# Performance work log

Hardware: AMD Instinct MI355X
Metric: run time of the kernel (lower is better)

## Reference

```python
import jax, jax.numpy as jnp
import numpy as np

B, S, D, Q = 8, 4096, 1024, 16  # batch, seq, embed_dim, n_qubits==ffn_dim


def setup_inputs() -> dict:
    key = jax.random.key(0)
    k = jax.random.split(key, 5)
    x = jax.random.normal(k[0], (B, S, D), dtype=jnp.float32)
    W1 = jax.random.normal(k[1], (D, Q), dtype=jnp.float32) * 0.02
    b1 = jnp.zeros((Q,), dtype=jnp.float32)
    theta = jax.random.normal(k[2], (Q,), dtype=jnp.float32)
    W2 = jax.random.normal(k[3], (Q, D), dtype=jnp.float32) * 0.02
    b2 = jnp.zeros((D,), dtype=jnp.float32)
    return {"x": x, "W1": W1, "b1": b1, "theta": theta, "W2": W2, "b2": b2}


def reference(x, W1, b1, theta, W2, b2):
    # linear1 + ReLU (dropout is identity in eval mode)
    h = jax.nn.relu(jnp.einsum("bsd,dq->bsq", x, W1) + b1)  # [B,S,Q] angles
    # QLayer: RY(h_i) then RY(theta_i) on wire i from |0>; rotations on the
    # same wire compose additively and <Z> after RY(a)|0> is cos(a), so
    # MeasureAll(PauliZ) == cos(h + theta) per wire (exact, product state).
    z = jnp.cos(h + theta)  # [B,S,Q]
    # linear2
    return jnp.einsum("bsq,qd->bsd", z, W2) + b2
```

## Files before the change

kernel.cpp:

```cpp
#include <hip/hip_runtime.h>
#include <math.h>
#include <stdint.h>

#define ROWS_TOTAL 32768
#define DDIM 1024
#define QDIM 16

typedef __attribute__((ext_vector_type(8))) short bf16x8;
typedef __attribute__((ext_vector_type(4))) float f32x4;

union ABfrag { uint32_t u[4]; bf16x8 v; };

__device__ __forceinline__ uint32_t packhi(uint32_t a, uint32_t b) {
  return __builtin_amdgcn_perm(b, a, 0x07060302u);
}

#define ZTPB 512
#define ZWPB 8
#define ZNBLOCKS (ROWS_TOTAL / 16)

__global__ __launch_bounds__(ZTPB, 4)
void z_kernel(const float* __restrict__ x, const float* __restrict__ W1,
              const float* __restrict__ b1, const float* __restrict__ theta,
              float* __restrict__ z, int zstride) {
  const int t    = threadIdx.x;
  const int lane = t & 63;
  const int wid  = t >> 6;
  const int g    = lane >> 4;
  const int q5   = lane & 15;

  __shared__ __align__(16) float red[ZWPB][64][4];

  const int row0 = blockIdx.x * 16;
  const int kb   = wid * 128;

  const float bq = b1[q5];
  const float tq = theta[q5];

  float wf[4][8];
#pragma unroll
  for (int s = 0; s < 4; ++s) {
    const float* wp = W1 + (size_t)(kb + 32 * s + 4 * g) * QDIM + q5;
#pragma unroll
    for (int j = 0; j < 4; ++j) wf[s][j] = wp[(size_t)j * QDIM];
#pragma unroll
    for (int j = 0; j < 4; ++j) wf[s][4 + j] = wp[(size_t)(16 + j) * QDIM];
  }

  const float* xl = x + (size_t)(row0 + q5) * DDIM + kb + 4 * g;
  float4 a0[4], a1[4];
#pragma unroll
  for (int s = 0; s < 4; ++s) {
    a0[s] = *reinterpret_cast<const float4*>(xl + 32 * s);
    a1[s] = *reinterpret_cast<const float4*>(xl + 32 * s + 16);
  }

  ABfrag bhi[4], blo[4];
#pragma unroll
  for (int s = 0; s < 4; ++s) {
    uint32_t u[8], lo[8];
#pragma unroll
    for (int j = 0; j < 8; ++j) {
      u[j]  = __float_as_uint(wf[s][j]);
      lo[j] = __float_as_uint(wf[s][j] - __uint_as_float(u[j] & 0xFFFF0000u));
    }
    bhi[s].u[0] = packhi(u[0], u[1]);   bhi[s].u[1] = packhi(u[2], u[3]);
    bhi[s].u[2] = packhi(u[4], u[5]);   bhi[s].u[3] = packhi(u[6], u[7]);
    blo[s].u[0] = packhi(lo[0], lo[1]); blo[s].u[1] = packhi(lo[2], lo[3]);
    blo[s].u[2] = packhi(lo[4], lo[5]); blo[s].u[3] = packhi(lo[6], lo[7]);
  }

  f32x4 acc = {0.f, 0.f, 0.f, 0.f};
#pragma unroll
  for (int s = 0; s < 4; ++s) {
    const float fv[8] = {a0[s].x, a0[s].y, a0[s].z, a0[s].w,
                         a1[s].x, a1[s].y, a1[s].z, a1[s].w};
    uint32_t u[8], lo[8];
#pragma unroll
    for (int j = 0; j < 8; ++j) {
      u[j]  = __float_as_uint(fv[j]);
      lo[j] = __float_as_uint(fv[j] - __uint_as_float(u[j] & 0xFFFF0000u));
    }
    ABfrag ahi, alo;
    ahi.u[0] = packhi(u[0], u[1]);   ahi.u[1] = packhi(u[2], u[3]);
    ahi.u[2] = packhi(u[4], u[5]);   ahi.u[3] = packhi(u[6], u[7]);
    alo.u[0] = packhi(lo[0], lo[1]); alo.u[1] = packhi(lo[2], lo[3]);
    alo.u[2] = packhi(lo[4], lo[5]); alo.u[3] = packhi(lo[6], lo[7]);

    acc = __builtin_amdgcn_mfma_f32_16x16x32_bf16(ahi.v, bhi[s].v, acc, 0, 0, 0);
    acc = __builtin_amdgcn_mfma_f32_16x16x32_bf16(alo.v, bhi[s].v, acc, 0, 0, 0);
    acc = __builtin_amdgcn_mfma_f32_16x16x32_bf16(ahi.v, blo[s].v, acc, 0, 0, 0);
  }

  *reinterpret_cast<f32x4*>(&red[wid][lane][0]) = acc;
  __syncthreads();

  if (wid == 0) {
    f32x4 s0 = *reinterpret_cast<const f32x4*>(&red[0][lane][0]);
#pragma unroll
    for (int w = 1; w < ZWPB; ++w)
      s0 += *reinterpret_cast<const f32x4*>(&red[w][lane][0]);

    const int r0 = g * 4;
#pragma unroll
    for (int i = 0; i < 4; ++i) {
      const float sv = fmaxf(s0[i] + bq, 0.f) + tq;
      z[(size_t)(row0 + r0 + i) * zstride + q5] = __cosf(sv);
    }
  }
}

#define OTPB 256
#define ORPB 16
#define ONBLOCKS (ROWS_TOTAL / ORPB)

__global__ __launch_bounds__(OTPB, 4)
void o_kernel(const float* z, int zstride, const float* __restrict__ W2,
              const float* __restrict__ b2, float* out) {
  const int t   = threadIdx.x;
  const int col = 4 * t;

  float4 w2r[QDIM];
#pragma unroll
  for (int q = 0; q < QDIM; ++q)
    w2r[q] = *reinterpret_cast<const float4*>(W2 + (size_t)q * DDIM + col);
  const float4 bb = *reinterpret_cast<const float4*>(b2 + col);

  const int row0 = blockIdx.x * ORPB;

  const float* zp0 = z + (size_t)row0 * zstride;
  float4 zc0 = *reinterpret_cast<const float4*>(zp0 + 0);
  float4 zc1 = *reinterpret_cast<const float4*>(zp0 + 4);
  float4 zc2 = *reinterpret_cast<const float4*>(zp0 + 8);
  float4 zc3 = *reinterpret_cast<const float4*>(zp0 + 12);

#pragma unroll
  for (int r = 0; r < ORPB; ++r) {
    float4 zn0 = zc0, zn1 = zc1, zn2 = zc2, zn3 = zc3;
    if (r + 1 < ORPB) {
      const float* znp = z + (size_t)(row0 + r + 1) * zstride;
      zn0 = *reinterpret_cast<const float4*>(znp + 0);
      zn1 = *reinterpret_cast<const float4*>(znp + 4);
      zn2 = *reinterpret_cast<const float4*>(znp + 8);
      zn3 = *reinterpret_cast<const float4*>(znp + 12);
    }

    const float zv[16] = {zc0.x, zc0.y, zc0.z, zc0.w,
                          zc1.x, zc1.y, zc1.z, zc1.w,
                          zc2.x, zc2.y, zc2.z, zc2.w,
                          zc3.x, zc3.y, zc3.z, zc3.w};
    float4 acc = bb;
#pragma unroll
    for (int q = 0; q < QDIM; ++q) {
      acc.x = fmaf(zv[q], w2r[q].x, acc.x);
      acc.y = fmaf(zv[q], w2r[q].y, acc.y);
      acc.z = fmaf(zv[q], w2r[q].z, acc.z);
      acc.w = fmaf(zv[q], w2r[q].w, acc.w);
    }
    *reinterpret_cast<float4*>(out + (size_t)(row0 + r) * DDIM + col) = acc;

    zc0 = zn0; zc1 = zn1; zc2 = zn2; zc3 = zn3;
  }
}

extern "C" void kernel_launch(void* const* d_in, const int* in_sizes, int n_in,
                              void* d_out, int out_size, void* d_ws, size_t ws_size,
                              hipStream_t stream) {
  const float* x     = (const float*)d_in[0];
  const float* W1    = (const float*)d_in[1];
  const float* b1    = (const float*)d_in[2];
  const float* theta = (const float*)d_in[3];
  const float* W2    = (const float*)d_in[4];
  const float* b2    = (const float*)d_in[5];
  float* out = (float*)d_out;

  const size_t zbytes = (size_t)ROWS_TOTAL * QDIM * sizeof(float);
  float* zbuf;
  int zstride;
  if (d_ws != nullptr && ws_size >= zbytes) {
    zbuf = (float*)d_ws;
    zstride = QDIM;
  } else {
    zbuf = out;
    zstride = DDIM;
  }

  z_kernel<<<dim3(ZNBLOCKS), dim3(ZTPB), 0, stream>>>(x, W1, b1, theta, zbuf, zstride);
  o_kernel<<<dim3(ONBLOCKS), dim3(OTPB), 0, stream>>>(zbuf, zstride, W2, b2, out);
}
```

Measured before the change: 55.46 us.

## Stage x tile through swizzled LDS for coalesced global loads in z_kernel

```diff
diff --git a/kernel.cpp b/kernel.cpp
--- a/kernel.cpp
+++ b/kernel.cpp
@@ -29,6 +29,7 @@
   const int g    = lane >> 4;
   const int q5   = lane & 15;
 
+  __shared__ __align__(16) float xs[16][DDIM];
   __shared__ __align__(16) float red[ZWPB][64][4];
 
   const int row0 = blockIdx.x * 16;
@@ -47,12 +48,27 @@
     for (int j = 0; j < 4; ++j) wf[s][4 + j] = wp[(size_t)(16 + j) * QDIM];
   }
 
-  const float* xl = x + (size_t)(row0 + q5) * DDIM + kb + 4 * g;
-  float4 a0[4], a1[4];
-#pragma unroll
-  for (int s = 0; s < 4; ++s) {
-    a0[s] = *reinterpret_cast<const float4*>(xl + 32 * s);
-    a1[s] = *reinterpret_cast<const float4*>(xl + 32 * s + 16);
+  float4 st[8];
+  {
+    const int rs = 2 * wid;
+#pragma unroll
+    for (int rr = 0; rr < 2; ++rr) {
+      const float* xp = x + (size_t)(row0 + rs + rr) * DDIM;
+#pragma unroll
+      for (int p = 0; p < 4; ++p)
+        st[rr * 4 + p] =
+            *reinterpret_cast<const float4*>(xp + 4 * (64 * p + lane));
+    }
+#pragma unroll
+    for (int rr = 0; rr < 2; ++rr) {
+      const int r = rs + rr;
+#pragma unroll
+      for (int p = 0; p < 4; ++p) {
+        const int u = 64 * p + lane;
+        *reinterpret_cast<float4*>(&xs[r][4 * (u ^ (r & 7))]) =
+            st[rr * 4 + p];
+      }
+    }
   }
 
   ABfrag bhi[4], blo[4];
@@ -68,6 +84,19 @@
     bhi[s].u[2] = packhi(u[4], u[5]);   bhi[s].u[3] = packhi(u[6], u[7]);
     blo[s].u[0] = packhi(lo[0], lo[1]); blo[s].u[1] = packhi(lo[2], lo[3]);
     blo[s].u[2] = packhi(lo[4], lo[5]); blo[s].u[3] = packhi(lo[6], lo[7]);
+  }
+
+  __syncthreads();
+
+  const int rr = lane & 15;
+  const int ub = 32 * wid;
+  float4 a0[4], a1[4];
+#pragma unroll
+  for (int s = 0; s < 4; ++s) {
+    a0[s] = *reinterpret_cast<const float4*>(
+        &xs[rr][4 * ((ub + 8 * s + g) ^ (rr & 7))]);
+    a1[s] = *reinterpret_cast<const float4*>(
+        &xs[rr][4 * ((ub + 8 * s + 4 + g) ^ (rr & 7))]);
   }
 
   f32x4 acc = {0.f, 0.f, 0.f, 0.f};
```

Measured after the change: 52.77 us. 4.8% less time.
